# Kernel tuning notes

Measured on AMD Instinct MI355X. Metric: run time of the kernel, lower is better.

## Reference

```python
import jax, jax.numpy as jnp
import numpy as np

INPUT_DIM = 16
NUM_MFS = 4
NUM_RULES = 1024
NUM_CLASSES = 10
BATCH = 4096


def setup_inputs() -> dict:
    key = jax.random.key(0)
    k1, k2, k3, k4, k5 = jax.random.split(key, 5)
    x = jax.random.normal(k1, (BATCH, INPUT_DIM), dtype=jnp.float32)
    centers = jax.random.normal(k2, (INPUT_DIM, NUM_MFS), dtype=jnp.float32)
    # widths must be positive (used as std of gaussian)
    widths = jax.random.uniform(k3, (INPUT_DIM, NUM_MFS), dtype=jnp.float32, minval=0.2, maxval=1.2)
    consequents = jax.random.normal(k4, (NUM_RULES, INPUT_DIM + 1, NUM_CLASSES), dtype=jnp.float32)
    rule_idx = jax.random.randint(k5, (INPUT_DIM, NUM_RULES), 0, NUM_MFS, dtype=jnp.int32)
    return {"x": x, "centers": centers, "widths": widths,
            "consequents": consequents, "rule_idx": rule_idx}


def reference(x, centers, widths, consequents, rule_idx):
    B, D = x.shape
    # Gaussian membership functions: [B, D, M]
    mfs = jnp.exp(-((x[:, :, None] - centers[None]) ** 2) / (2.0 * widths[None] ** 2) + 1e-9)
    # Gather rule-specific memberships: [B, D, R]
    d_idx = jnp.arange(D)[:, None]  # [D, 1] broadcasts with rule_idx [D, R]
    rule_mfs = mfs[:, d_idx, rule_idx]
    # Firing strengths (product over input dims) and normalization: [B, R]
    firing = jnp.prod(rule_mfs, axis=1)
    norm_fs = firing / (jnp.sum(firing, axis=1, keepdims=True) + 1e-9)
    # Extended input with bias column: [B, D+1]
    x_ext = jnp.concatenate([x, jnp.ones((B, 1), dtype=x.dtype)], axis=1)
    # phi = norm_fs[:, :, None] * x_ext[:, None, :]; y = phi_flat @ beta_flat
    # expressed as a single contraction (same math, phi is detached w.r.t. x_ext)
    y_hat = jnp.einsum('br,bi,ric->bc', norm_fs, jax.lax.stop_gradient(x_ext), consequents)
    return y_hat, norm_fs, x_ext
```

## Files before the change

kernel.cpp:

```cpp
#include <hip/hip_runtime.h>

#define B 4096
#define D 16
#define R 1024
#define NC 10
#define IC 170
#define NT 11
#define NP 176
#define KC 64
#define KSPLIT 4
#define RPB (R / KSPLIT)
#define BT 16
#define BSTR 72
#define GSP 192

typedef __attribute__((ext_vector_type(8))) short short8;
typedef __attribute__((ext_vector_type(4))) float f32x4;

__device__ __forceinline__ unsigned short f2bf(float f) {
    unsigned u = __float_as_uint(f);
    return (unsigned short)((u + 0x7fffu + ((u >> 16) & 1u)) >> 16);
}

__global__ void pack_rules(const int* __restrict__ rule_idx, unsigned* __restrict__ packed) {
    int r = blockIdx.x * 256 + threadIdx.x;
    unsigned bits = 0;
#pragma unroll
    for (int d = 0; d < D; ++d)
        bits |= (((unsigned)rule_idx[d * R + r]) & 3u) << (2 * d);
    packed[r] = bits;
}

__global__ __launch_bounds__(256) void convert_b(const float* __restrict__ cons,
                                                 unsigned short* __restrict__ Bsw) {
    int t = blockIdx.x * 256 + threadIdx.x;
    int row = t >> 10;
    int k   = t & 1023;
    float v = (row < IC) ? cons[(size_t)k * IC + row] : 0.0f;
    Bsw[t] = f2bf(v);
}

__global__ __launch_bounds__(256) void firing_kernel(
    const float* __restrict__ x, const float* __restrict__ centers,
    const float* __restrict__ widths, const unsigned* __restrict__ packed,
    float* __restrict__ out_norm, float* __restrict__ out_xext,
    float* __restrict__ out_y)
{
    __shared__ float s_z[64];
    __shared__ float s_z2[8][16];
    __shared__ float s_z4[4 * 256];
    __shared__ float s_red[8];
    const int b = blockIdx.x, tid = threadIdx.x;

    if (b < (B * NC) / 256) out_y[b * 256 + tid] = 0.0f;

    if (tid < 64) {
        int d = tid >> 2;
        float xv = x[b * D + d];
        float c = centers[tid], w = widths[tid];
        float diff = xv - c;
        s_z[tid] = 1e-9f - diff * diff / (2.0f * w * w);
    }
    if (tid < 17) out_xext[b * 17 + tid] = (tid < 16) ? x[b * D + tid] : 1.0f;
    __syncthreads();
    if (tid < 128) {
        int p = tid >> 4, i = tid & 15;
        s_z2[p][i] = s_z[p * 8 + (i & 3)] + s_z[p * 8 + 4 + ((i >> 2) & 3)];
    }
    __syncthreads();
#pragma unroll
    for (int q = 0; q < 4; ++q)
        s_z4[q * 256 + tid] = s_z2[2 * q][tid & 15] + s_z2[2 * q + 1][(tid >> 4) & 15];
    __syncthreads();

    float f[4], lsum = 0.0f;
#pragma unroll
    for (int j = 0; j < 4; ++j) {
        unsigned w = packed[tid + 256 * j];
        float s = s_z4[w & 255] + s_z4[256 + ((w >> 8) & 255)]
                + s_z4[512 + ((w >> 16) & 255)] + s_z4[768 + (w >> 24)];
        f[j] = __expf(s);
        lsum += f[j];
    }
#pragma unroll
    for (int off = 1; off < 64; off <<= 1) lsum += __shfl_xor(lsum, off, 64);
    const int lane = tid & 63, wid = tid >> 6;
    if (lane == 0) s_red[wid] = lsum;
    __syncthreads();
    if (tid == 0) {
        float tot = s_red[0] + s_red[1] + s_red[2] + s_red[3] + 1e-9f;
        s_red[4] = 1.0f / tot;
    }
    __syncthreads();
    const float inv = s_red[4];
#pragma unroll
    for (int j = 0; j < 4; ++j)
        out_norm[(size_t)b * R + tid + 256 * j] = f[j] * inv;
}

__global__ __launch_bounds__(256, 4) void yhat_kernel(
    const float* __restrict__ norm, const unsigned short* __restrict__ Bsw,
    const float* __restrict__ x, float* __restrict__ out_y)
{
    __shared__ unsigned short Bs[NT * 16 * BSTR];
    __shared__ unsigned short As[BT * BSTR];
    __shared__ float xe[BT * 17];

    const int tid = threadIdx.x;
    const int mt = blockIdx.x & 255;
    const int ks = blockIdx.x >> 8;
    const int bl0 = mt * BT;
    const int r_base = ks * RPB;

    for (int t = tid; t < BT * 17; t += 256) {
        int bl = t / 17, i = t - bl * 17;
        xe[t] = (i < 16) ? x[(size_t)(bl0 + bl) * D + i] : 1.0f;
    }

    const int lane = tid & 63, wv = tid >> 6;
    const int m_ = lane & 15, q_ = lane >> 4;
    const int nt0 = wv * 3;
    const int ntn = (wv == 3) ? 2 : 3;

    f32x4 acc[3];
    const f32x4 zf = {0.f, 0.f, 0.f, 0.f};
    acc[0] = zf; acc[1] = zf; acc[2] = zf;

    for (int c0 = 0; c0 < RPB; c0 += KC) {
        const int kabs = r_base + c0;
        __syncthreads();
        for (int t = tid; t < NP * 8; t += 256) {
            int row = t >> 3, seg = t & 7;
            *(short8*)&Bs[row * BSTR + seg * 8] =
                *(const short8*)&Bsw[row * R + kabs + seg * 8];
        }
        {
            int row = tid >> 4, c4 = tid & 15;
            float4 v = *(const float4*)&norm[(size_t)(bl0 + row) * R + kabs + c4 * 4];
            ushort4 o;
            o.x = f2bf(v.x); o.y = f2bf(v.y); o.z = f2bf(v.z); o.w = f2bf(v.w);
            *(ushort4*)&As[row * BSTR + c4 * 4] = o;
        }
        __syncthreads();
#pragma unroll
        for (int kh = 0; kh < 2; ++kh) {
            short8 a = *(const short8*)&As[m_ * BSTR + kh * 32 + q_ * 8];
#pragma unroll
            for (int j = 0; j < 3; ++j) {
                if (j < ntn) {
                    int nt = nt0 + j;
                    short8 bfrag = *(const short8*)&Bs[(nt * 16 + m_) * BSTR + kh * 32 + q_ * 8];
                    acc[j] = __builtin_amdgcn_mfma_f32_16x16x32_bf16(a, bfrag, acc[j], 0, 0, 0);
                }
            }
        }
    }

    __syncthreads();
    float* Gs = (float*)Bs;
#pragma unroll
    for (int j = 0; j < 3; ++j) {
        if (j < ntn) {
            int nt = nt0 + j;
#pragma unroll
            for (int r = 0; r < 4; ++r)
                Gs[(q_ * 4 + r) * GSP + nt * 16 + m_] = acc[j][r];
        }
    }
    __syncthreads();
    if (tid < BT * NC) {
        int bl = tid / NC, c = tid - bl * NC;
        float y = 0.0f;
#pragma unroll
        for (int i = 0; i < 17; ++i)
            y += xe[bl * 17 + i] * Gs[bl * GSP + i * NC + c];
        atomicAdd(&out_y[(size_t)(bl0 + bl) * NC + c], y);
    }
}

extern "C" void kernel_launch(void* const* d_in, const int* in_sizes, int n_in,
                              void* d_out, int out_size, void* d_ws, size_t ws_size,
                              hipStream_t stream) {
    const float* x        = (const float*)d_in[0];
    const float* centers  = (const float*)d_in[1];
    const float* widths   = (const float*)d_in[2];
    const float* cons     = (const float*)d_in[3];
    const int*   rule_idx = (const int*)d_in[4];

    float* out      = (float*)d_out;
    float* out_y    = out;
    float* out_norm = out + (size_t)B * NC;
    float* out_xext = out + (size_t)B * NC + (size_t)B * R;

    unsigned* packed     = (unsigned*)d_ws;
    unsigned short* Bsw  = (unsigned short*)((char*)d_ws + 4096);

    pack_rules<<<R / 256, 256, 0, stream>>>(rule_idx, packed);
    convert_b<<<(NP * R) / 256, 256, 0, stream>>>(cons, Bsw);
    firing_kernel<<<B, 256, 0, stream>>>(x, centers, widths, packed,
                                         out_norm, out_xext, out_y);
    yhat_kernel<<<(B / BT) * KSPLIT, 256, 0, stream>>>(out_norm, Bsw, x, out_y);
}
```

Measured before the change: 94.43 us.

## Enlarge yhat batch tile to 64 rows and merge prep kernels into one launch

The y_hat GEMM now gives each block 64 batch rows and 128 rules (KSPLIT 8). It loads the whole A and B slice into shared memory once and reuses each B fragment across four MFMA row blocks, replacing the 64-wide K-chunk loop that had two barriers per step. The per-rule packing, consequent conversion and out_y zeroing are merged into a single prep kernel, removing one launch. The trade-off is more shared memory and registers per block (launch bounds lowered to 2 blocks per SM), 512 blocks instead of 1024, and more atomic contention across the eight K splits.

Result: faster. 91.99 us (-2.6%).

```diff
diff --git a/kernel.cpp b/kernel.cpp
--- a/kernel.cpp
+++ b/kernel.cpp
@@ -7,12 +7,11 @@
 #define IC 170
 #define NT 11
 #define NP 176
-#define KC 64
-#define KSPLIT 4
+#define KSPLIT 8
 #define RPB (R / KSPLIT)
-#define BT 16
-#define BSTR 72
-#define GSP 192
+#define BT 64
+#define BSTR 136
+#define GSP 180
 
 typedef __attribute__((ext_vector_type(8))) short short8;
 typedef __attribute__((ext_vector_type(4))) float f32x4;
@@ -22,29 +21,34 @@
     return (unsigned short)((u + 0x7fffu + ((u >> 16) & 1u)) >> 16);
 }
 
-__global__ void pack_rules(const int* __restrict__ rule_idx, unsigned* __restrict__ packed) {
-    int r = blockIdx.x * 256 + threadIdx.x;
-    unsigned bits = 0;
-#pragma unroll
-    for (int d = 0; d < D; ++d)
-        bits |= (((unsigned)rule_idx[d * R + r]) & 3u) << (2 * d);
-    packed[r] = bits;
-}
-
-__global__ __launch_bounds__(256) void convert_b(const float* __restrict__ cons,
-                                                 unsigned short* __restrict__ Bsw) {
-    int t = blockIdx.x * 256 + threadIdx.x;
-    int row = t >> 10;
-    int k   = t & 1023;
-    float v = (row < IC) ? cons[(size_t)k * IC + row] : 0.0f;
-    Bsw[t] = f2bf(v);
+__global__ __launch_bounds__(256) void prep_kernel(
+    const float* __restrict__ cons, unsigned short* __restrict__ Bsw,
+    const int* __restrict__ rule_idx, unsigned* __restrict__ packed,
+    float* __restrict__ out_y)
+{
+    const int bid = blockIdx.x, tid = threadIdx.x;
+    if (bid < 704) {
+        int t = bid * 256 + tid;
+        int row = t >> 10;
+        int k   = t & 1023;
+        float v = (row < IC) ? cons[(size_t)k * IC + row] : 0.0f;
+        Bsw[t] = f2bf(v);
+    } else if (bid < 708) {
+        int r = (bid - 704) * 256 + tid;
+        unsigned bits = 0;
+#pragma unroll
+        for (int d = 0; d < D; ++d)
+            bits |= (((unsigned)rule_idx[d * R + r]) & 3u) << (2 * d);
+        packed[r] = bits;
+    } else {
+        out_y[(bid - 708) * 256 + tid] = 0.0f;
+    }
 }
 
 __global__ __launch_bounds__(256) void firing_kernel(
     const float* __restrict__ x, const float* __restrict__ centers,
     const float* __restrict__ widths, const unsigned* __restrict__ packed,
-    float* __restrict__ out_norm, float* __restrict__ out_xext,
-    float* __restrict__ out_y)
+    float* __restrict__ out_norm, float* __restrict__ out_xext)
 {
     __shared__ float s_z[64];
     __shared__ float s_z2[8][16];
@@ -52,8 +56,6 @@
     __shared__ float s_red[8];
     const int b = blockIdx.x, tid = threadIdx.x;
 
-    if (b < (B * NC) / 256) out_y[b * 256 + tid] = 0.0f;
-
     if (tid < 64) {
         int d = tid >> 2;
         float xv = x[b * D + d];
@@ -98,60 +100,63 @@
         out_norm[(size_t)b * R + tid + 256 * j] = f[j] * inv;
 }
 
-__global__ __launch_bounds__(256, 4) void yhat_kernel(
+__global__ __launch_bounds__(256, 2) void yhat_kernel(
     const float* __restrict__ norm, const unsigned short* __restrict__ Bsw,
     const float* __restrict__ x, float* __restrict__ out_y)
 {
-    __shared__ unsigned short Bs[NT * 16 * BSTR];
+    __shared__ unsigned short Bs[NP * BSTR];
     __shared__ unsigned short As[BT * BSTR];
     __shared__ float xe[BT * 17];
 
     const int tid = threadIdx.x;
-    const int mt = blockIdx.x & 255;
-    const int ks = blockIdx.x >> 8;
+    const int mt = blockIdx.x & 63;
+    const int ks = blockIdx.x >> 6;
     const int bl0 = mt * BT;
-    const int r_base = ks * RPB;
+    const int kabs = ks * RPB;
 
     for (int t = tid; t < BT * 17; t += 256) {
         int bl = t / 17, i = t - bl * 17;
         xe[t] = (i < 16) ? x[(size_t)(bl0 + bl) * D + i] : 1.0f;
     }
+    for (int t = tid; t < NP * 16; t += 256) {
+        int row = t >> 4, seg = t & 15;
+        *(short8*)&Bs[row * BSTR + seg * 8] =
+            *(const short8*)&Bsw[row * R + kabs + seg * 8];
+    }
+    for (int t = tid; t < BT * 32; t += 256) {
+        int row = t >> 5, c4 = t & 31;
+        float4 v = *(const float4*)&norm[(size_t)(bl0 + row) * R + kabs + c4 * 4];
+        ushort4 o;
+        o.x = f2bf(v.x); o.y = f2bf(v.y); o.z = f2bf(v.z); o.w = f2bf(v.w);
+        *(ushort4*)&As[row * BSTR + c4 * 4] = o;
+    }
+    __syncthreads();
 
     const int lane = tid & 63, wv = tid >> 6;
     const int m_ = lane & 15, q_ = lane >> 4;
     const int nt0 = wv * 3;
     const int ntn = (wv == 3) ? 2 : 3;
 
-    f32x4 acc[3];
+    f32x4 acc[4][3];
     const f32x4 zf = {0.f, 0.f, 0.f, 0.f};
-    acc[0] = zf; acc[1] = zf; acc[2] = zf;
-
-    for (int c0 = 0; c0 < RPB; c0 += KC) {
-        const int kabs = r_base + c0;
-        __syncthreads();
-        for (int t = tid; t < NP * 8; t += 256) {
-            int row = t >> 3, seg = t & 7;
-            *(short8*)&Bs[row * BSTR + seg * 8] =
-                *(const short8*)&Bsw[row * R + kabs + seg * 8];
-        }
-        {
-            int row = tid >> 4, c4 = tid & 15;
-            float4 v = *(const float4*)&norm[(size_t)(bl0 + row) * R + kabs + c4 * 4];
-            ushort4 o;
-            o.x = f2bf(v.x); o.y = f2bf(v.y); o.z = f2bf(v.z); o.w = f2bf(v.w);
-            *(ushort4*)&As[row * BSTR + c4 * 4] = o;
-        }
-        __syncthreads();
-#pragma unroll
-        for (int kh = 0; kh < 2; ++kh) {
-            short8 a = *(const short8*)&As[m_ * BSTR + kh * 32 + q_ * 8];
-#pragma unroll
-            for (int j = 0; j < 3; ++j) {
-                if (j < ntn) {
-                    int nt = nt0 + j;
-                    short8 bfrag = *(const short8*)&Bs[(nt * 16 + m_) * BSTR + kh * 32 + q_ * 8];
-                    acc[j] = __builtin_amdgcn_mfma_f32_16x16x32_bf16(a, bfrag, acc[j], 0, 0, 0);
-                }
+#pragma unroll
+    for (int mb = 0; mb < 4; ++mb)
+#pragma unroll
+        for (int j = 0; j < 3; ++j) acc[mb][j] = zf;
+
+#pragma unroll
+    for (int kh = 0; kh < 4; ++kh) {
+        short8 a[4];
+#pragma unroll
+        for (int mb = 0; mb < 4; ++mb)
+            a[mb] = *(const short8*)&As[(mb * 16 + m_) * BSTR + kh * 32 + q_ * 8];
+#pragma unroll
+        for (int j = 0; j < 3; ++j) {
+            if (j < ntn) {
+                short8 bfrag = *(const short8*)&Bs[((nt0 + j) * 16 + m_) * BSTR + kh * 32 + q_ * 8];
+#pragma unroll
+                for (int mb = 0; mb < 4; ++mb)
+                    acc[mb][j] = __builtin_amdgcn_mfma_f32_16x16x32_bf16(a[mb], bfrag, acc[mb][j], 0, 0, 0);
             }
         }
     }
@@ -163,13 +168,15 @@
         if (j < ntn) {
             int nt = nt0 + j;
 #pragma unroll
-            for (int r = 0; r < 4; ++r)
-                Gs[(q_ * 4 + r) * GSP + nt * 16 + m_] = acc[j][r];
+            for (int mb = 0; mb < 4; ++mb)
+#pragma unroll
+                for (int r = 0; r < 4; ++r)
+                    Gs[(mb * 16 + q_ * 4 + r) * GSP + nt * 16 + m_] = acc[mb][j][r];
         }
     }
     __syncthreads();
-    if (tid < BT * NC) {
-        int bl = tid / NC, c = tid - bl * NC;
+    for (int t = tid; t < BT * NC; t += 256) {
+        int bl = t / NC, c = t - bl * NC;
         float y = 0.0f;
 #pragma unroll
         for (int i = 0; i < 17; ++i)
@@ -195,9 +202,8 @@
     unsigned* packed     = (unsigned*)d_ws;
     unsigned short* Bsw  = (unsigned short*)((char*)d_ws + 4096);
 
-    pack_rules<<<R / 256, 256, 0, stream>>>(rule_idx, packed);
-    convert_b<<<(NP * R) / 256, 256, 0, stream>>>(cons, Bsw);
+    prep_kernel<<<868, 256, 0, stream>>>(cons, Bsw, rule_idx, packed, out_y);
     firing_kernel<<<B, 256, 0, stream>>>(x, centers, widths, packed,
-                                         out_norm, out_xext, out_y);
+                                         out_norm, out_xext);
     yhat_kernel<<<(B / BT) * KSPLIT, 256, 0, stream>>>(out_norm, Bsw, x, out_y);
 }
```
